# Kernel optimization log

Hardware: AMD Instinct MI355X
Metric: run time of the kernel (lower is better)

Reference implementation:

```python
import jax, jax.numpy as jnp
import numpy as np

N_NODES = 100000
N_EDGES = 800000
D = 32           # output_dim == node feature dim
D_EDGE = 32      # embedded edge feature dim
H = 64           # psi hidden units
PSI_IN = 4 * D + D_EDGE  # 160


def setup_inputs() -> dict:
    key = jax.random.key(0)
    ks = jax.random.split(key, 12)
    inp = {
        "h_d_prev": jax.random.normal(ks[0], (N_NODES, D), dtype=jnp.float32),
        "h_s": jax.random.normal(ks[1], (N_NODES, D), dtype=jnp.float32),
        "edge_features_embedded": jax.random.normal(ks[2], (N_EDGES, D_EDGE), dtype=jnp.float32),
        "sender_indices": jax.random.randint(ks[3], (N_EDGES,), 0, N_NODES, dtype=jnp.int32),
        "receiver_indices": jax.random.randint(ks[4], (N_EDGES,), 0, N_NODES, dtype=jnp.int32),
        # psi MLP params (Dense with relu on every layer, incl. last since final_activation=None)
        "psi_w0": jax.random.normal(ks[5], (PSI_IN, H), dtype=jnp.float32) * (1.0 / np.sqrt(PSI_IN)),
        "psi_b0": jnp.zeros((H,), dtype=jnp.float32),
        "psi_w1": jax.random.normal(ks[6], (H, H), dtype=jnp.float32) * (1.0 / np.sqrt(H)),
        "psi_b1": jnp.zeros((H,), dtype=jnp.float32),
        "psi_w2": jax.random.normal(ks[7], (H, D), dtype=jnp.float32) * (1.0 / np.sqrt(H)),
        "psi_b2": jnp.zeros((D,), dtype=jnp.float32),
        # final W matrix (Dense, no bias)
        "W": jax.random.normal(ks[8], (D, D), dtype=jnp.float32) * (1.0 / np.sqrt(D)),
    }
    return inp


def reference(h_d_prev, h_s, edge_features_embedded, sender_indices, receiver_indices,
              psi_w0, psi_b0, psi_w1, psi_b1, psi_w2, psi_b2, W):
    # Gather node features onto edges
    h_di = h_d_prev[sender_indices]      # [E, D]
    h_dj = h_d_prev[receiver_indices]    # [E, D]
    h_si = h_s[sender_indices]           # [E, D]
    h_sj = h_s[receiver_indices]         # [E, D]

    psi_in = jnp.concatenate([h_si, h_sj, h_di, h_dj, edge_features_embedded], axis=-1)  # [E, 4D+De]
    x = jax.nn.relu(psi_in @ psi_w0 + psi_b0)
    x = jax.nn.relu(x @ psi_w1 + psi_b1)
    psi_out = jax.nn.relu(x @ psi_w2 + psi_b2)  # [E, D]

    s_ij = psi_out * (h_dj - h_di)  # [E, D]
    aggregated = jax.ops.segment_sum(s_ij, receiver_indices, num_segments=h_d_prev.shape[0])  # [N, D]
    return h_d_prev + aggregated @ W
```

## Files before the change

### kernel.cpp

```cpp
#include <hip/hip_runtime.h>

#define DD 32
#define HH 64

typedef __attribute__((ext_vector_type(8))) short bf16x8;
typedef __attribute__((ext_vector_type(4))) float f32x4;

static __device__ __forceinline__ unsigned short f2bf(float x) {
    union { float f; unsigned u; } v; v.f = x;
    unsigned r = (v.u + 0x7FFFu + ((v.u >> 16) & 1u)) >> 16;
    return (unsigned short)r;
}

__global__ __launch_bounds__(256) void prep_weights(
    const float* __restrict__ w0, const float* __restrict__ w1,
    const float* __restrict__ w2, unsigned short* __restrict__ frags)
{
    const int tid = blockIdx.x * 256 + threadIdx.x;
    const int f = tid >> 6, l = tid & 63;
    if (f >= 32) return;
    const int c = l & 15, q = l >> 4;
    unsigned short* dst = frags + f * 512 + l * 8;
    if (f < 20) {
        const int kk = f >> 2, t = f & 3;
        const int n = t * 16 + c, kb = kk * 32 + q * 8;
        #pragma unroll
        for (int j = 0; j < 8; ++j) dst[j] = f2bf(w0[(kb + j) * HH + n]);
    } else if (f < 28) {
        const int f2 = f - 20, kk = f2 >> 2, t = f2 & 3;
        const int n = t * 16 + c, kb = kk * 32 + q * 8;
        #pragma unroll
        for (int j = 0; j < 8; ++j) dst[j] = f2bf(w1[(kb + j) * HH + n]);
    } else {
        const int f3 = f - 28, kk = f3 >> 1, t = f3 & 1;
        const int n = t * 16 + c, kb = kk * 32 + q * 8;
        #pragma unroll
        for (int j = 0; j < 8; ++j) dst[j] = f2bf(w2[(kb + j) * DD + n]);
    }
}

__global__ __launch_bounds__(256, 2) void edge_mfma(
    const float* __restrict__ h_d, const float* __restrict__ h_s,
    const float* __restrict__ ef,
    const int* __restrict__ snd, const int* __restrict__ rcv,
    const unsigned short* __restrict__ frags,
    const float* __restrict__ b0, const float* __restrict__ b1,
    const float* __restrict__ b2,
    float* __restrict__ agg, int E, int ntiles)
{
    __shared__ __align__(16) unsigned short xbuf[4][2][16 * 72];

    const int lane = threadIdx.x & 63;
    const int w = threadIdx.x >> 6;
    const int c = lane & 15, q = lane >> 4;

    bf16x8 wf[32];
    #pragma unroll
    for (int f = 0; f < 32; ++f)
        wf[f] = *(const bf16x8*)(frags + f * 512 + lane * 8);

    const float b0t[4] = {b0[c], b0[16 + c], b0[32 + c], b0[48 + c]};
    const float b1t[4] = {b1[c], b1[16 + c], b1[32 + c], b1[48 + c]};
    const float b2t[2] = {b2[c], b2[16 + c]};

    unsigned short* xb1 = xbuf[w][0];
    unsigned short* xb2 = xbuf[w][1];

    const int wave_id = blockIdx.x * 4 + w;
    const int nwaves = gridDim.x * 4;

    for (int tile = wave_id; tile < ntiles; tile += nwaves) {
        const int base = tile * 16;
        int e = base + c; if (e >= E) e = E - 1;
        const int si = snd[e], ri = rcv[e];
        const float* srcs[5] = { h_s + (size_t)si * DD, h_s + (size_t)ri * DD,
                                 h_d + (size_t)si * DD, h_d + (size_t)ri * DD,
                                 ef  + (size_t)e  * DD };

        f32x4 c0[4] = {f32x4{0,0,0,0}, f32x4{0,0,0,0}, f32x4{0,0,0,0}, f32x4{0,0,0,0}};
        #pragma unroll
        for (int kk = 0; kk < 5; ++kk) {
            const float* s = srcs[kk] + q * 8;
            const float4 v0 = ((const float4*)s)[0];
            const float4 v1 = ((const float4*)s)[1];
            bf16x8 a;
            a[0] = (short)f2bf(v0.x); a[1] = (short)f2bf(v0.y);
            a[2] = (short)f2bf(v0.z); a[3] = (short)f2bf(v0.w);
            a[4] = (short)f2bf(v1.x); a[5] = (short)f2bf(v1.y);
            a[6] = (short)f2bf(v1.z); a[7] = (short)f2bf(v1.w);
            #pragma unroll
            for (int t = 0; t < 4; ++t)
                c0[t] = __builtin_amdgcn_mfma_f32_16x16x32_bf16(a, wf[kk * 4 + t], c0[t], 0, 0, 0);
        }
        #pragma unroll
        for (int t = 0; t < 4; ++t) {
            #pragma unroll
            for (int r = 0; r < 4; ++r) {
                const float v = fmaxf(c0[t][r] + b0t[t], 0.0f);
                xb1[(q * 4 + r) * 72 + t * 16 + c] = f2bf(v);
            }
        }

        f32x4 c1[4] = {f32x4{0,0,0,0}, f32x4{0,0,0,0}, f32x4{0,0,0,0}, f32x4{0,0,0,0}};
        #pragma unroll
        for (int kk = 0; kk < 2; ++kk) {
            const bf16x8 a = *(const bf16x8*)(xb1 + c * 72 + kk * 32 + q * 8);
            #pragma unroll
            for (int t = 0; t < 4; ++t)
                c1[t] = __builtin_amdgcn_mfma_f32_16x16x32_bf16(a, wf[20 + kk * 4 + t], c1[t], 0, 0, 0);
        }
        #pragma unroll
        for (int t = 0; t < 4; ++t) {
            #pragma unroll
            for (int r = 0; r < 4; ++r) {
                const float v = fmaxf(c1[t][r] + b1t[t], 0.0f);
                xb2[(q * 4 + r) * 72 + t * 16 + c] = f2bf(v);
            }
        }

        f32x4 c2[2] = {f32x4{0,0,0,0}, f32x4{0,0,0,0}};
        #pragma unroll
        for (int kk = 0; kk < 2; ++kk) {
            const bf16x8 a = *(const bf16x8*)(xb2 + c * 72 + kk * 32 + q * 8);
            #pragma unroll
            for (int t = 0; t < 2; ++t)
                c2[t] = __builtin_amdgcn_mfma_f32_16x16x32_bf16(a, wf[28 + kk * 2 + t], c2[t], 0, 0, 0);
        }

        int erv[4], sir[4], rir[4];
        #pragma unroll
        for (int r = 0; r < 4; ++r) {
            const int ee = base + q * 4 + r;
            erv[r] = ee;
            const int eec = ee < E ? ee : E - 1;
            sir[r] = snd[eec]; rir[r] = rcv[eec];
        }
        #pragma unroll
        for (int t = 0; t < 2; ++t) {
            const int h = t * 16 + c;
            #pragma unroll
            for (int r = 0; r < 4; ++r) {
                if (erv[r] < E) {
                    const float psi = fmaxf(c2[t][r] + b2t[t], 0.0f);
                    const float d = h_d[(size_t)rir[r] * DD + h] - h_d[(size_t)sir[r] * DD + h];
                    atomicAdd(agg + (size_t)rir[r] * DD + h, psi * d);
                }
            }
        }
    }
}

__global__ __launch_bounds__(256) void out_kernel(
    const float* __restrict__ h_d, const float* __restrict__ agg,
    const float* __restrict__ W, float* __restrict__ out, int N)
{
    const int idx = blockIdx.x * 256 + threadIdx.x;
    if (idx >= N * DD) return;
    const int n = idx >> 5;
    const int d = idx & 31;
    const float* arow = agg + (size_t)n * DD;
    float s = h_d[idx];
    #pragma unroll
    for (int k = 0; k < DD; ++k) s = fmaf(arow[k], W[k * DD + d], s);
    out[idx] = s;
}

extern "C" void kernel_launch(void* const* d_in, const int* in_sizes, int n_in,
                              void* d_out, int out_size, void* d_ws, size_t ws_size,
                              hipStream_t stream) {
    const float* h_d = (const float*)d_in[0];
    const float* h_s = (const float*)d_in[1];
    const float* ef  = (const float*)d_in[2];
    const int*   snd = (const int*)d_in[3];
    const int*   rcv = (const int*)d_in[4];
    const float* w0  = (const float*)d_in[5];
    const float* b0  = (const float*)d_in[6];
    const float* w1  = (const float*)d_in[7];
    const float* b1  = (const float*)d_in[8];
    const float* w2  = (const float*)d_in[9];
    const float* b2  = (const float*)d_in[10];
    const float* W   = (const float*)d_in[11];
    float* out = (float*)d_out;

    const int N = in_sizes[0] / DD;
    const int E = in_sizes[3];
    const int ntiles = (E + 15) / 16;

    float* agg = (float*)d_ws;
    unsigned short* frags = (unsigned short*)((char*)d_ws + (size_t)N * DD * sizeof(float));

    hipMemsetAsync(agg, 0, (size_t)N * DD * sizeof(float), stream);
    prep_weights<<<8, 256, 0, stream>>>(w0, w1, w2, frags);
    edge_mfma<<<1024, 256, 0, stream>>>(h_d, h_s, ef, snd, rcv, frags,
                                        b0, b1, b2, agg, E, ntiles);
    out_kernel<<<((N * DD) + 255) / 256, 256, 0, stream>>>(h_d, agg, W, out, N);
}
```

Measured before the change: 366.0 us.

## Stage weights in LDS, prefetch indices, reuse gathered h_d differences via LDS

Moves most of the bf16 MLP weight fragments from per-lane registers into shared memory, which cuts VGPR pressure and allows 512-thread blocks at a higher occupancy bound. It also prefetches the next tile's sender and receiver indices, issues all ten gathers up front, and keeps the h_d difference and receiver ids in LDS so the epilogue no longer re-gathers from global memory. The cost is extra LDS reads of weight fragments on every MFMA and more LDS use overall, plus a single shared activation buffer per wave.

New measurement: 446.6 us. 1.22x slower.

```diff
diff --git a/kernel.cpp b/kernel.cpp
--- a/kernel.cpp
+++ b/kernel.cpp
@@ -2,6 +2,9 @@
 
 #define DD 32
 #define HH 64
+
+#define XSTR 72
+#define DSTR 33
 
 typedef __attribute__((ext_vector_type(8))) short bf16x8;
 typedef __attribute__((ext_vector_type(4))) float f32x4;
@@ -39,7 +42,7 @@
     }
 }
 
-__global__ __launch_bounds__(256, 2) void edge_mfma(
+__global__ __launch_bounds__(512, 4) void edge_mfma(
     const float* __restrict__ h_d, const float* __restrict__ h_s,
     const float* __restrict__ ef,
     const int* __restrict__ snd, const int* __restrict__ rcv,
@@ -48,101 +51,138 @@
     const float* __restrict__ b2,
     float* __restrict__ agg, int E, int ntiles)
 {
-    __shared__ __align__(16) unsigned short xbuf[4][2][16 * 72];
+    __shared__ __align__(16) unsigned short wlds[28 * 512];
+    __shared__ __align__(16) unsigned short xbuf[8][16 * XSTR];
+    __shared__ float hdiff[8][16 * DSTR];
+    __shared__ int rcvb[8][16];
 
     const int lane = threadIdx.x & 63;
     const int w = threadIdx.x >> 6;
     const int c = lane & 15, q = lane >> 4;
 
-    bf16x8 wf[32];
+    for (int i = threadIdx.x; i < 28 * 512 / 8; i += 512)
+        ((float4*)wlds)[i] = ((const float4*)frags)[i];
+    bf16x8 wf2[4];
     #pragma unroll
-    for (int f = 0; f < 32; ++f)
-        wf[f] = *(const bf16x8*)(frags + f * 512 + lane * 8);
+    for (int t = 0; t < 4; ++t)
+        wf2[t] = *(const bf16x8*)(frags + (28 + t) * 512 + lane * 8);
+    __syncthreads();
 
     const float b0t[4] = {b0[c], b0[16 + c], b0[32 + c], b0[48 + c]};
     const float b1t[4] = {b1[c], b1[16 + c], b1[32 + c], b1[48 + c]};
     const float b2t[2] = {b2[c], b2[16 + c]};
 
-    unsigned short* xb1 = xbuf[w][0];
-    unsigned short* xb2 = xbuf[w][1];
-
-    const int wave_id = blockIdx.x * 4 + w;
-    const int nwaves = gridDim.x * 4;
+    unsigned short* xb = xbuf[w];
+    float* hd = hdiff[w];
+    int* rb = rcvb[w];
+
+    const int wave_id = blockIdx.x * 8 + w;
+    const int nwaves = gridDim.x * 8;
+
+    int nsi = 0, nri = 0;
+    if (wave_id < ntiles) {
+        int e0 = wave_id * 16 + c; if (e0 >= E) e0 = E - 1;
+        nsi = snd[e0]; nri = rcv[e0];
+    }
 
     for (int tile = wave_id; tile < ntiles; tile += nwaves) {
         const int base = tile * 16;
+        const int si = nsi, ri = nri;
+        {
+            const int nt = tile + nwaves;
+            if (nt < ntiles) {
+                int e2 = nt * 16 + c; if (e2 >= E) e2 = E - 1;
+                nsi = snd[e2]; nri = rcv[e2];
+            }
+        }
         int e = base + c; if (e >= E) e = E - 1;
-        const int si = snd[e], ri = rcv[e];
-        const float* srcs[5] = { h_s + (size_t)si * DD, h_s + (size_t)ri * DD,
-                                 h_d + (size_t)si * DD, h_d + (size_t)ri * DD,
-                                 ef  + (size_t)e  * DD };
+
+        const float* ps = h_s + (size_t)si * DD + q * 8;
+        const float* pr = h_s + (size_t)ri * DD + q * 8;
+        const float* qs = h_d + (size_t)si * DD + q * 8;
+        const float* qr = h_d + (size_t)ri * DD + q * 8;
+        const float* pe = ef  + (size_t)e  * DD + q * 8;
+        float4 g[10];
+        g[0] = ((const float4*)ps)[0]; g[1] = ((const float4*)ps)[1];
+        g[2] = ((const float4*)pr)[0]; g[3] = ((const float4*)pr)[1];
+        g[4] = ((const float4*)qs)[0]; g[5] = ((const float4*)qs)[1];
+        g[6] = ((const float4*)qr)[0]; g[7] = ((const float4*)qr)[1];
+        g[8] = ((const float4*)pe)[0]; g[9] = ((const float4*)pe)[1];
+
+        hd[c * DSTR + q * 8 + 0] = g[6].x - g[4].x;
+        hd[c * DSTR + q * 8 + 1] = g[6].y - g[4].y;
+        hd[c * DSTR + q * 8 + 2] = g[6].z - g[4].z;
+        hd[c * DSTR + q * 8 + 3] = g[6].w - g[4].w;
+        hd[c * DSTR + q * 8 + 4] = g[7].x - g[5].x;
+        hd[c * DSTR + q * 8 + 5] = g[7].y - g[5].y;
+        hd[c * DSTR + q * 8 + 6] = g[7].z - g[5].z;
+        hd[c * DSTR + q * 8 + 7] = g[7].w - g[5].w;
+        if (q == 0) rb[c] = ri;
 
         f32x4 c0[4] = {f32x4{0,0,0,0}, f32x4{0,0,0,0}, f32x4{0,0,0,0}, f32x4{0,0,0,0}};
         #pragma unroll
         for (int kk = 0; kk < 5; ++kk) {
-            const float* s = srcs[kk] + q * 8;
-            const float4 v0 = ((const float4*)s)[0];
-            const float4 v1 = ((const float4*)s)[1];
+            const float4 v0 = g[2 * kk], v1 = g[2 * kk + 1];
             bf16x8 a;
             a[0] = (short)f2bf(v0.x); a[1] = (short)f2bf(v0.y);
             a[2] = (short)f2bf(v0.z); a[3] = (short)f2bf(v0.w);
             a[4] = (short)f2bf(v1.x); a[5] = (short)f2bf(v1.y);
             a[6] = (short)f2bf(v1.z); a[7] = (short)f2bf(v1.w);
             #pragma unroll
-            for (int t = 0; t < 4; ++t)
-                c0[t] = __builtin_amdgcn_mfma_f32_16x16x32_bf16(a, wf[kk * 4 + t], c0[t], 0, 0, 0);
+            for (int t = 0; t < 4; ++t) {
+                const bf16x8 b = *(const bf16x8*)(wlds + (kk * 4 + t) * 512 + lane * 8);
+                c0[t] = __builtin_amdgcn_mfma_f32_16x16x32_bf16(a, b, c0[t], 0, 0, 0);
+            }
         }
         #pragma unroll
         for (int t = 0; t < 4; ++t) {
             #pragma unroll
             for (int r = 0; r < 4; ++r) {
                 const float v = fmaxf(c0[t][r] + b0t[t], 0.0f);
-                xb1[(q * 4 + r) * 72 + t * 16 + c] = f2bf(v);
+                xb[(q * 4 + r) * XSTR + t * 16 + c] = f2bf(v);
             }
         }
 
         f32x4 c1[4] = {f32x4{0,0,0,0}, f32x4{0,0,0,0}, f32x4{0,0,0,0}, f32x4{0,0,0,0}};
         #pragma unroll
         for (int kk = 0; kk < 2; ++kk) {
-            const bf16x8 a = *(const bf16x8*)(xb1 + c * 72 + kk * 32 + q * 8);
-            #pragma unroll
-            for (int t = 0; t < 4; ++t)
-                c1[t] = __builtin_amdgcn_mfma_f32_16x16x32_bf16(a, wf[20 + kk * 4 + t], c1[t], 0, 0, 0);
+            const bf16x8 a = *(const bf16x8*)(xb + c * XSTR + kk * 32 + q * 8);
+            #pragma unroll
+            for (int t = 0; t < 4; ++t) {
+                const bf16x8 b = *(const bf16x8*)(wlds + (20 + kk * 4 + t) * 512 + lane * 8);
+                c1[t] = __builtin_amdgcn_mfma_f32_16x16x32_bf16(a, b, c1[t], 0, 0, 0);
+            }
         }
         #pragma unroll
         for (int t = 0; t < 4; ++t) {
             #pragma unroll
             for (int r = 0; r < 4; ++r) {
                 const float v = fmaxf(c1[t][r] + b1t[t], 0.0f);
-                xb2[(q * 4 + r) * 72 + t * 16 + c] = f2bf(v);
+                xb[(q * 4 + r) * XSTR + t * 16 + c] = f2bf(v);
             }
         }
 
         f32x4 c2[2] = {f32x4{0,0,0,0}, f32x4{0,0,0,0}};
         #pragma unroll
         for (int kk = 0; kk < 2; ++kk) {
-            const bf16x8 a = *(const bf16x8*)(xb2 + c * 72 + kk * 32 + q * 8);
+            const bf16x8 a = *(const bf16x8*)(xb + c * XSTR + kk * 32 + q * 8);
             #pragma unroll
             for (int t = 0; t < 2; ++t)
-                c2[t] = __builtin_amdgcn_mfma_f32_16x16x32_bf16(a, wf[28 + kk * 2 + t], c2[t], 0, 0, 0);
-        }
-
-        int erv[4], sir[4], rir[4];
-        #pragma unroll
-        for (int r = 0; r < 4; ++r) {
-            const int ee = base + q * 4 + r;
-            erv[r] = ee;
-            const int eec = ee < E ? ee : E - 1;
-            sir[r] = snd[eec]; rir[r] = rcv[eec];
-        }
+                c2[t] = __builtin_amdgcn_mfma_f32_16x16x32_bf16(a, wf2[kk * 2 + t], c2[t], 0, 0, 0);
+        }
+
+        int rir[4];
+        #pragma unroll
+        for (int r = 0; r < 4; ++r) rir[r] = rb[q * 4 + r];
         #pragma unroll
         for (int t = 0; t < 2; ++t) {
             const int h = t * 16 + c;
             #pragma unroll
             for (int r = 0; r < 4; ++r) {
-                if (erv[r] < E) {
+                const int ee = base + q * 4 + r;
+                if (ee < E) {
                     const float psi = fmaxf(c2[t][r] + b2t[t], 0.0f);
-                    const float d = h_d[(size_t)rir[r] * DD + h] - h_d[(size_t)sir[r] * DD + h];
+                    const float d = hd[(q * 4 + r) * DSTR + h];
                     atomicAdd(agg + (size_t)rir[r] * DD + h, psi * d);
                 }
             }
@@ -191,7 +231,7 @@
 
     hipMemsetAsync(agg, 0, (size_t)N * DD * sizeof(float), stream);
     prep_weights<<<8, 256, 0, stream>>>(w0, w1, w2, frags);
-    edge_mfma<<<1024, 256, 0, stream>>>(h_d, h_s, ef, snd, rcv, frags,
-                                        b0, b1, b2, agg, E, ntiles);
+    edge_mfma<<<512, 512, 0, stream>>>(h_d, h_s, ef, snd, rcv, frags,
+                                       b0, b1, b2, agg, E, ntiles);
     out_kernel<<<((N * DD) + 255) / 256, 256, 0, stream>>>(h_d, agg, W, out, N);
 }
```
